# Kernel tuning notes

Hardware: AMD Instinct MI355X
Metric: run time of the kernel (lower is better)

The kernel has to match this reference:

```python
import jax, jax.numpy as jnp
import numpy as np

B, L, D, H, DH, FF = 4, 1024, 1024, 16, 64, 4096
EPS = 1e-5


def _layer_norm(x, g, b):
    m = jnp.mean(x, -1, keepdims=True)
    v = jnp.mean((x - m) ** 2, -1, keepdims=True)
    return (x - m) * jax.lax.rsqrt(v + EPS) * g + b


def setup_inputs() -> dict:
    key = jax.random.key(0)
    ks = jax.random.split(key, 20)
    s = 0.02  # param init scale
    return {
        "x": jax.random.normal(ks[0], (B, L, D), jnp.float32),
        "adj_mask_matrix": jax.random.uniform(ks[1], (B * H, L, L), jnp.float32),
        "com_mask_matrix": jax.random.uniform(ks[2], (B * H, L, L), jnp.float32),
        "lattice_rel": jax.random.normal(ks[3], (2, 1, 1, DH), jnp.float32),
        "Wq": jax.random.normal(ks[4], (D, D), jnp.float32) * s,
        "bq": jnp.zeros((D,), jnp.float32),
        "Wk": jax.random.normal(ks[5], (D, D), jnp.float32) * s,
        "bk": jnp.zeros((D,), jnp.float32),
        "Wv": jax.random.normal(ks[6], (D, D), jnp.float32) * s,
        "bv": jnp.zeros((D,), jnp.float32),
        "Wo": jax.random.normal(ks[7], (D, D), jnp.float32) * s,
        "bo": jnp.zeros((D,), jnp.float32),
        "ln1_scale": jnp.ones((D,), jnp.float32),
        "ln1_bias": jnp.zeros((D,), jnp.float32),
        "W1": jax.random.normal(ks[8], (D, FF), jnp.float32) * s,
        "b1": jnp.zeros((FF,), jnp.float32),
        "W2": jax.random.normal(ks[9], (FF, D), jnp.float32) * s,
        "b2": jnp.zeros((D,), jnp.float32),
        "ln2_scale": jnp.ones((D,), jnp.float32),
        "ln2_bias": jnp.zeros((D,), jnp.float32),
    }


def reference(x, adj_mask_matrix, com_mask_matrix, lattice_rel,
              Wq, bq, Wk, bk, Wv, bv, Wo, bo, ln1_scale, ln1_bias,
              W1, b1, W2, b2, ln2_scale, ln2_bias):
    Bsz, Ln, Dm = x.shape
    # QKV projections; flat reshape [B,L,H*dh] -> [B*H,L,dh] matches torch .view
    Q = (x @ Wq + bq).reshape(Bsz * H, Ln, DH)
    K = (x @ Wk + bk).reshape(Bsz * H, Ln, DH)
    V = (x @ Wv + bv).reshape(Bsz * H, Ln, DH)
    scale = DH ** (-0.5)
    adj_rel = lattice_rel[0]  # [1,1,dh] broadcasts over (B*H, L)
    com_rel = lattice_rel[1]
    att_adj = jnp.einsum('bqd,bkd->bqk', Q + adj_rel, K + adj_rel) * scale
    att_com = jnp.einsum('bqd,bkd->bqk', Q + com_rel, K + com_rel) * scale
    # post-softmax multiplicative masking, then sum of the two attention maps
    mask_att = (jax.nn.softmax(att_adj, axis=-1) * adj_mask_matrix
                + jax.nn.softmax(att_com, axis=-1) * com_mask_matrix)
    context = jnp.matmul(mask_att, V).reshape(Bsz, Ln, H * DH)
    out = _layer_norm(context @ Wo + bo + x, ln1_scale, ln1_bias)
    ff = jax.nn.relu(out @ W1 + b1) @ W2 + b2
    return _layer_norm(ff + out, ln2_scale, ln2_bias)
```

## Files before the change

kernel.cpp:

```cpp
#include <hip/hip_runtime.h>
#include <hip/hip_bf16.h>

typedef __attribute__((ext_vector_type(8))) short s16x8;
typedef __attribute__((ext_vector_type(4))) float f32x4;
typedef unsigned short u16;
typedef unsigned int u32;

__device__ __forceinline__ u16 f2b(float f) {
    u32 u = __float_as_uint(f);
    u32 r = (u + 0x7fffu + ((u >> 16) & 1u)) >> 16;
    return (u16)r;
}
__device__ __forceinline__ u16 bfbits(float f) {
    __hip_bfloat16 h = __float2bfloat16(f);
    return *reinterpret_cast<u16*>(&h);
}

#define MFMA16(a, b, c) __builtin_amdgcn_mfma_f32_16x16x32_bf16(a, b, c, 0, 0, 0)
#define GLDS(gp, lp)                                                              \
    __builtin_amdgcn_global_load_lds((const __attribute__((address_space(1))) void*)(gp), \
                                     (__attribute__((address_space(3))) void*)(lp), 16, 0, 0)

__global__ void k_f2b(const float* __restrict__ in, u16* __restrict__ out, int n4) {
    int i = blockIdx.x * 256 + threadIdx.x;
    if (i >= n4) return;
    float4 v = ((const float4*)in)[i];
    ushort4 o;
    o.x = f2b(v.x); o.y = f2b(v.y); o.z = f2b(v.z); o.w = f2b(v.w);
    ((ushort4*)out)[i] = o;
}

__global__ void k_wtrans(const float* __restrict__ W, u16* __restrict__ Wt, int K, int N) {
    __shared__ float t[32][33];
    int bx = blockIdx.x * 32, by = blockIdx.y * 32;
    int tx = threadIdx.x, ty = threadIdx.y;
    for (int i = 0; i < 32; i += 8)
        t[ty + i][tx] = W[(size_t)(by + ty + i) * N + bx + tx];
    __syncthreads();
    for (int i = 0; i < 32; i += 8)
        Wt[(size_t)(bx + ty + i) * K + by + tx] = f2b(t[tx][ty + i]);
}

template <int EPI>
__global__ __launch_bounds__(256) void gemm_bt(const u16* __restrict__ A, const u16* __restrict__ Bt,
                                               void* __restrict__ Cv, int M, int N, int K,
                                               const float* __restrict__ bias) {
    __shared__ __align__(16) short lA[128 * 64];
    __shared__ __align__(16) short lB[128 * 64];
    const int tid = threadIdx.x, lane = tid & 63, w = tid >> 6;
    const int l15 = lane & 15, lg = lane >> 4;
    const int bm = blockIdx.y, bn = blockIdx.x;
    const int wr = w >> 1, wc = w & 1;
    const int m0 = bm * 128, n0 = bn * 128;
    f32x4 acc[4][4] = {};

    for (int k0 = 0; k0 < K; k0 += 64) {
        #pragma unroll
        for (int i = 0; i < 4; i++) {
            int chunk = w * 4 + i;
            int arow = m0 + chunk * 8 + (lane >> 3);
            GLDS(A + (size_t)arow * K + k0 + (lane & 7) * 8, (short*)lA + chunk * 512);
            int brow = n0 + chunk * 8 + (lane >> 3);
            GLDS(Bt + (size_t)brow * K + k0 + (lane & 7) * 8, (short*)lB + chunk * 512);
        }
        __syncthreads();
        #pragma unroll
        for (int ks = 0; ks < 2; ks++) {
            s16x8 af[4], bfr[4];
            #pragma unroll
            for (int m = 0; m < 4; m++)
                af[m] = *(const s16x8*)&lA[(wr * 64 + m * 16 + l15) * 64 + ks * 32 + lg * 8];
            #pragma unroll
            for (int n = 0; n < 4; n++)
                bfr[n] = *(const s16x8*)&lB[(wc * 64 + n * 16 + l15) * 64 + ks * 32 + lg * 8];
            #pragma unroll
            for (int m = 0; m < 4; m++)
                #pragma unroll
                for (int n = 0; n < 4; n++)
                    acc[m][n] = MFMA16(af[m], bfr[n], acc[m][n]);
        }
        __syncthreads();
    }
    const int rbase = m0 + wr * 64, cbase = n0 + wc * 64;
    #pragma unroll
    for (int m = 0; m < 4; m++)
        #pragma unroll
        for (int n = 0; n < 4; n++) {
            int col = cbase + n * 16 + l15;
            int row0 = rbase + m * 16 + lg * 4;
            if (EPI == 0) {
                float* C = (float*)Cv;
                #pragma unroll
                for (int r = 0; r < 4; r++)
                    C[(size_t)(row0 + r) * N + col] = acc[m][n][r];
            } else {
                u16* C = (u16*)Cv;
                float bv = bias[col];
                #pragma unroll
                for (int r = 0; r < 4; r++)
                    C[(size_t)(row0 + r) * N + col] = bfbits(fmaxf(acc[m][n][r] + bv, 0.f));
            }
        }
}

__global__ __launch_bounds__(256) void gemm_bt64(const u16* __restrict__ A, const u16* __restrict__ Bt,
                                                 float* __restrict__ C, int M, int N, int K) {
    __shared__ __align__(16) short lA[128 * 64];
    __shared__ __align__(16) short lB[64 * 64];
    const int tid = threadIdx.x, lane = tid & 63, w = tid >> 6;
    const int l15 = lane & 15, lg = lane >> 4;
    const int m0 = blockIdx.y * 128, n0 = blockIdx.x * 64;
    f32x4 acc[2][4] = {};

    for (int k0 = 0; k0 < K; k0 += 64) {
        #pragma unroll
        for (int i = 0; i < 4; i++) {
            int chunk = w * 4 + i;
            int arow = m0 + chunk * 8 + (lane >> 3);
            GLDS(A + (size_t)arow * K + k0 + (lane & 7) * 8, (short*)lA + chunk * 512);
        }
        #pragma unroll
        for (int i = 0; i < 2; i++) {
            int chunk = w * 2 + i;
            int brow = n0 + chunk * 8 + (lane >> 3);
            GLDS(Bt + (size_t)brow * K + k0 + (lane & 7) * 8, (short*)lB + chunk * 512);
        }
        __syncthreads();
        #pragma unroll
        for (int ks = 0; ks < 2; ks++) {
            s16x8 af[2], bfr[4];
            #pragma unroll
            for (int m = 0; m < 2; m++)
                af[m] = *(const s16x8*)&lA[(w * 32 + m * 16 + l15) * 64 + ks * 32 + lg * 8];
            #pragma unroll
            for (int n = 0; n < 4; n++)
                bfr[n] = *(const s16x8*)&lB[(n * 16 + l15) * 64 + ks * 32 + lg * 8];
            #pragma unroll
            for (int m = 0; m < 2; m++)
                #pragma unroll
                for (int n = 0; n < 4; n++)
                    acc[m][n] = MFMA16(af[m], bfr[n], acc[m][n]);
        }
        __syncthreads();
    }
    #pragma unroll
    for (int m = 0; m < 2; m++)
        #pragma unroll
        for (int n = 0; n < 4; n++) {
            int col = n0 + n * 16 + l15;
            int row0 = m0 + w * 32 + m * 16 + lg * 4;
            #pragma unroll
            for (int r = 0; r < 4; r++)
                C[(size_t)(row0 + r) * N + col] = acc[m][n][r];
        }
}

__global__ void k_epi_qk2(const float* __restrict__ QKVf, int coff, const float* __restrict__ bias,
                          const float* __restrict__ rel, u16* __restrict__ Pa, u16* __restrict__ Pc, int n4) {
    int i = blockIdx.x * 256 + threadIdx.x;
    if (i >= n4) return;
    int f = i * 4;
    int row = f >> 10, col = f & 1023;
    float4 v = *(const float4*)(QKVf + (size_t)row * 3072 + coff + col);
    int d = f & 63;
    float4 b = *(const float4*)(bias + col);
    float4 r0 = *(const float4*)(rel + d);
    float4 r1 = *(const float4*)(rel + 64 + d);
    ushort4 oa, oc;
    oa.x = f2b(v.x + b.x + r0.x); oa.y = f2b(v.y + b.y + r0.y);
    oa.z = f2b(v.z + b.z + r0.z); oa.w = f2b(v.w + b.w + r0.w);
    oc.x = f2b(v.x + b.x + r1.x); oc.y = f2b(v.y + b.y + r1.y);
    oc.z = f2b(v.z + b.z + r1.z); oc.w = f2b(v.w + b.w + r1.w);
    ((ushort4*)Pa)[i] = oa;
    ((ushort4*)Pc)[i] = oc;
}

__global__ void k_vtrans2(const float* __restrict__ QKVf, const float* __restrict__ bv, u16* __restrict__ Vt) {
    __shared__ float t[64][65];
    const int g = blockIdx.y, lt = blockIdx.x;
    const int tx = threadIdx.x & 63, ty = threadIdx.x >> 6;
    const size_t gQ = (size_t)g * 65536;
    for (int i = 0; i < 64; i += 4) {
        int l = lt * 64 + ty + i;
        size_t f = gQ + (size_t)l * 64 + tx;
        t[ty + i][tx] = QKVf[(f >> 10) * 3072 + 2048 + (f & 1023)] + bv[f & 1023];
    }
    __syncthreads();
    for (int i = 0; i < 64; i += 4) {
        int d = ty + i;
        Vt[gQ + (size_t)d * 1024 + lt * 64 + tx] = f2b(t[tx][d]);
    }
}

__global__ __launch_bounds__(256) void k_attn1(const u16* __restrict__ Qa, const u16* __restrict__ Qc,
                                               const u16* __restrict__ Ka, const u16* __restrict__ Kc,
                                               const u16* __restrict__ Vt,
                                               const float* __restrict__ adjm, const float* __restrict__ comm,
                                               float* __restrict__ ctxA, float* __restrict__ ctxC) {
    const int g = blockIdx.y, qt = blockIdx.x, s = blockIdx.z;
    const u16* __restrict__ Q = s ? Qc : Qa;
    const u16* __restrict__ K = s ? Kc : Ka;
    const float* __restrict__ mask = s ? comm : adjm;
    float* __restrict__ ctxp = s ? ctxC : ctxA;

    const int tid = threadIdx.x, lane = tid & 63, w = tid >> 6;
    const int l15 = lane & 15, lg = lane >> 4;
    __shared__ __align__(16) float lE[4][16][68];

    const int q0 = qt * 64 + w * 16;
    const size_t gQ = (size_t)g * 65536;
    const float* __restrict__ mrow = mask + (size_t)g * 1048576 + (size_t)(q0 + l15) * 1024;
    const float scale = 0.125f;

    s16x8 qf[2];
    #pragma unroll
    for (int ks = 0; ks < 2; ks++)
        qf[ks] = *(const s16x8*)(Q + gQ + (size_t)(q0 + l15) * 64 + ks * 32 + lg * 8);

    f32x4 ca[4] = {};
    float la[4] = {0.f, 0.f, 0.f, 0.f};

    float4 mc[2][2], mn[2][2];
    #pragma unroll
    for (int ks = 0; ks < 2; ks++) {
        const float* p = mrow + ks * 32 + lg * 8;
        mc[ks][0] = *(const float4*)p;
        mc[ks][1] = *(const float4*)(p + 4);
    }

    #pragma unroll 2
    for (int kb = 0; kb < 1024; kb += 64) {
        const int kbn = (kb + 64) & 1023;
        #pragma unroll
        for (int ks = 0; ks < 2; ks++) {
            const float* p = mrow + kbn + ks * 32 + lg * 8;
            mn[ks][0] = *(const float4*)p;
            mn[ks][1] = *(const float4*)(p + 4);
        }
        f32x4 sa[4] = {};
        #pragma unroll
        for (int ks = 0; ks < 2; ks++)
            #pragma unroll
            for (int n = 0; n < 4; n++) {
                s16x8 kf = *(const s16x8*)(K + gQ + (size_t)(kb + n * 16 + l15) * 64 + ks * 32 + lg * 8);
                sa[n] = MFMA16(qf[ks], kf, sa[n]);
            }
        #pragma unroll
        for (int n = 0; n < 4; n++)
            #pragma unroll
            for (int r = 0; r < 4; r++) {
                float e = __expf(sa[n][r] * scale);
                la[r] += e;
                lE[w][lg * 4 + r][n * 16 + l15] = e;
            }
        #pragma unroll
        for (int ks = 0; ks < 2; ks++) {
            const float* ep = &lE[w][l15][ks * 32 + lg * 8];
            float4 e0 = *(const float4*)ep, e1 = *(const float4*)(ep + 4);
            union { s16x8 v; u16 u[8]; } pf;
            pf.u[0] = bfbits(e0.x * mc[ks][0].x); pf.u[1] = bfbits(e0.y * mc[ks][0].y);
            pf.u[2] = bfbits(e0.z * mc[ks][0].z); pf.u[3] = bfbits(e0.w * mc[ks][0].w);
            pf.u[4] = bfbits(e1.x * mc[ks][1].x); pf.u[5] = bfbits(e1.y * mc[ks][1].y);
            pf.u[6] = bfbits(e1.z * mc[ks][1].z); pf.u[7] = bfbits(e1.w * mc[ks][1].w);
            #pragma unroll
            for (int d = 0; d < 4; d++) {
                s16x8 vf = *(const s16x8*)(Vt + gQ + (size_t)(d * 16 + l15) * 1024 + kb + ks * 32 + lg * 8);
                ca[d] = MFMA16(pf.v, vf, ca[d]);
            }
        }
        #pragma unroll
        for (int ks = 0; ks < 2; ks++) {
            mc[ks][0] = mn[ks][0];
            mc[ks][1] = mn[ks][1];
        }
    }
    #pragma unroll
    for (int r = 0; r < 4; r++)
        #pragma unroll
        for (int m = 8; m >= 1; m >>= 1)
            la[r] += __shfl_xor(la[r], m);
    #pragma unroll
    for (int r = 0; r < 4; r++) {
        float il = 1.f / la[r];
        int row = q0 + lg * 4 + r;
        #pragma unroll
        for (int d = 0; d < 4; d++)
            ctxp[gQ + (size_t)row * 64 + d * 16 + l15] = ca[d][r] * il;
    }
}

__global__ void k_comb(const float* __restrict__ A, const float* __restrict__ C,
                       u16* __restrict__ out, int n4) {
    int i = blockIdx.x * 256 + threadIdx.x;
    if (i >= n4) return;
    float4 a = ((const float4*)A)[i];
    float4 c = ((const float4*)C)[i];
    ushort4 o;
    o.x = f2b(a.x + c.x); o.y = f2b(a.y + c.y);
    o.z = f2b(a.z + c.z); o.w = f2b(a.w + c.w);
    ((ushort4*)out)[i] = o;
}

__global__ __launch_bounds__(256) void k_ln(const float* __restrict__ a, const float* __restrict__ bias,
                                            const float* __restrict__ resid, const float* __restrict__ gamma,
                                            const float* __restrict__ beta, float* __restrict__ out,
                                            u16* __restrict__ outb) {
    const int row = blockIdx.x, tid = threadIdx.x;
    const size_t base = (size_t)row * 1024 + tid * 4;
    float4 av = *(const float4*)(a + base);
    float4 rv = *(const float4*)(resid + base);
    float4 bv = *(const float4*)(bias + tid * 4);
    float t0 = av.x + rv.x + bv.x, t1 = av.y + rv.y + bv.y;
    float t2 = av.z + rv.z + bv.z, t3 = av.w + rv.w + bv.w;
    __shared__ float red[4];
    float s = t0 + t1 + t2 + t3;
    #pragma unroll
    for (int m = 32; m >= 1; m >>= 1) s += __shfl_xor(s, m);
    int w = tid >> 6;
    if ((tid & 63) == 0) red[w] = s;
    __syncthreads();
    float mean = (red[0] + red[1] + red[2] + red[3]) * (1.f / 1024.f);
    float d0 = t0 - mean, d1 = t1 - mean, d2 = t2 - mean, d3 = t3 - mean;
    float q = d0 * d0 + d1 * d1 + d2 * d2 + d3 * d3;
    __syncthreads();
    #pragma unroll
    for (int m = 32; m >= 1; m >>= 1) q += __shfl_xor(q, m);
    if ((tid & 63) == 0) red[w] = q;
    __syncthreads();
    float var = (red[0] + red[1] + red[2] + red[3]) * (1.f / 1024.f);
    float rs = rsqrtf(var + 1e-5f);
    float4 gv = *(const float4*)(gamma + tid * 4);
    float4 bev = *(const float4*)(beta + tid * 4);
    float o0 = d0 * rs * gv.x + bev.x, o1 = d1 * rs * gv.y + bev.y;
    float o2 = d2 * rs * gv.z + bev.z, o3 = d3 * rs * gv.w + bev.w;
    *(float4*)(out + base) = make_float4(o0, o1, o2, o3);
    if (outb) {
        ushort4 ob;
        ob.x = f2b(o0); ob.y = f2b(o1); ob.z = f2b(o2); ob.w = f2b(o3);
        *(ushort4*)(outb + base) = ob;
    }
}

extern "C" void kernel_launch(void* const* d_in, const int* in_sizes, int n_in,
                              void* d_out, int out_size, void* d_ws, size_t ws_size,
                              hipStream_t stream) {
    const float* x    = (const float*)d_in[0];
    const float* adjm = (const float*)d_in[1];
    const float* comm = (const float*)d_in[2];
    const float* rel  = (const float*)d_in[3];
    const float* Wq   = (const float*)d_in[4];
    const float* bq   = (const float*)d_in[5];
    const float* Wk   = (const float*)d_in[6];
    const float* bk   = (const float*)d_in[7];
    const float* Wv   = (const float*)d_in[8];
    const float* bv   = (const float*)d_in[9];
    const float* Wo   = (const float*)d_in[10];
    const float* bo   = (const float*)d_in[11];
    const float* g1   = (const float*)d_in[12];
    const float* be1  = (const float*)d_in[13];
    const float* W1   = (const float*)d_in[14];
    const float* b1   = (const float*)d_in[15];
    const float* W2   = (const float*)d_in[16];
    const float* b2   = (const float*)d_in[17];
    const float* g2   = (const float*)d_in[18];
    const float* be2  = (const float*)d_in[19];
    float* out = (float*)d_out;

    char* ws = (char*)d_ws;
    const size_t MB = 1048576;
    u16*   xb    = (u16*)(ws + 0 * MB);
    u16*   Wqkvt = (u16*)(ws + 8 * MB);
    u16*   Wot   = (u16*)(ws + 14 * MB);
    u16*   W1t   = (u16*)(ws + 16 * MB);
    u16*   W2t   = (u16*)(ws + 24 * MB);
    float* QKVf  = (float*)(ws + 32 * MB);
    u16*   Qab   = (u16*)(ws + 80 * MB);
    u16*   Qcb   = (u16*)(ws + 88 * MB);
    u16*   Kab   = (u16*)(ws + 96 * MB);
    u16*   Kcb   = (u16*)(ws + 104 * MB);
    u16*   Vtb   = (u16*)(ws + 112 * MB);
    float* ctxA  = (float*)(ws + 120 * MB);
    float* ctxC  = (float*)(ws + 136 * MB);
    u16*   ctx   = (u16*)(ws + 152 * MB);
    float* ctxWo = (float*)(ws + 32 * MB);
    float* out1  = (float*)(ws + 48 * MB);
    u16*   out1b = (u16*)(ws + 64 * MB);
    u16*   rb    = (u16*)(ws + 80 * MB);
    float* ff2   = (float*)(ws + 0 * MB);

    dim3 tb(32, 8);
    k_f2b<<<4096, 256, 0, stream>>>(x, xb, 1048576);
    k_wtrans<<<dim3(32, 32), tb, 0, stream>>>(Wq, Wqkvt, 1024, 1024);
    k_wtrans<<<dim3(32, 32), tb, 0, stream>>>(Wk, Wqkvt + 1024 * 1024, 1024, 1024);
    k_wtrans<<<dim3(32, 32), tb, 0, stream>>>(Wv, Wqkvt + 2 * 1024 * 1024, 1024, 1024);
    k_wtrans<<<dim3(32, 32), tb, 0, stream>>>(Wo, Wot, 1024, 1024);
    k_wtrans<<<dim3(128, 32), tb, 0, stream>>>(W1, W1t, 1024, 4096);
    k_wtrans<<<dim3(32, 128), tb, 0, stream>>>(W2, W2t, 4096, 1024);
    gemm_bt<0><<<dim3(24, 32), 256, 0, stream>>>(xb, Wqkvt, QKVf, 4096, 3072, 1024, nullptr);
    k_epi_qk2<<<4096, 256, 0, stream>>>(QKVf, 0, bq, rel, Qab, Qcb, 1048576);
    k_epi_qk2<<<4096, 256, 0, stream>>>(QKVf, 1024, bk, rel, Kab, Kcb, 1048576);
    k_vtrans2<<<dim3(16, 64), 256, 0, stream>>>(QKVf, bv, Vtb);
    k_attn1<<<dim3(16, 64, 2), 256, 0, stream>>>(Qab, Qcb, Kab, Kcb, Vtb, adjm, comm, ctxA, ctxC);
    k_comb<<<4096, 256, 0, stream>>>(ctxA, ctxC, ctx, 1048576);
    gemm_bt64<<<dim3(16, 32), 256, 0, stream>>>(ctx, Wot, ctxWo, 4096, 1024, 1024);
    k_ln<<<4096, 256, 0, stream>>>(ctxWo, bo, x, g1, be1, out1, out1b);
    gemm_bt<1><<<dim3(32, 32), 256, 0, stream>>>(out1b, W1t, rb, 4096, 4096, 1024, b1);
    gemm_bt64<<<dim3(16, 32), 256, 0, stream>>>(rb, W2t, ff2, 4096, 1024, 4096);
    k_ln<<<4096, 256, 0, stream>>>(ff2, b2, out1, g2, be2, out, nullptr);
}
```

Baseline: 657.7 us.

## Split attention into QK-exp and masked PV kernels with bf16 score buffer

Splits the fused attention kernel into two passes per branch. The first computes exp(QK^T) and row sums, storing exp scores as bf16 in a 128MB workspace. The second reads them back, applies the fp32 mask, and runs the PV MFMA. The second branch's PV pass folds in the adj/com sum and bf16 conversion, removing the separate combine kernel. It also remaps block ids so heads are grouped per XCD. The aim is to decouple mask streaming from the QK compute, but it adds a large round trip of score traffic and extra bf16 rounding of the exp values.

Measured after the change: 670.6 us. About the same (+1.9%).

```diff
diff --git a/kernel.cpp b/kernel.cpp
--- a/kernel.cpp
+++ b/kernel.cpp
@@ -14,6 +14,9 @@
 __device__ __forceinline__ u16 bfbits(float f) {
     __hip_bfloat16 h = __float2bfloat16(f);
     return *reinterpret_cast<u16*>(&h);
+}
+__device__ __forceinline__ float b2f(u16 b) {
+    return __uint_as_float(((u32)b) << 16);
 }
 
 #define MFMA16(a, b, c) __builtin_amdgcn_mfma_f32_16x16x32_bf16(a, b, c, 0, 0, 0)
@@ -192,24 +195,18 @@
     }
 }
 
-__global__ __launch_bounds__(256) void k_attn1(const u16* __restrict__ Qa, const u16* __restrict__ Qc,
-                                               const u16* __restrict__ Ka, const u16* __restrict__ Kc,
-                                               const u16* __restrict__ Vt,
-                                               const float* __restrict__ adjm, const float* __restrict__ comm,
-                                               float* __restrict__ ctxA, float* __restrict__ ctxC) {
-    const int g = blockIdx.y, qt = blockIdx.x, s = blockIdx.z;
-    const u16* __restrict__ Q = s ? Qc : Qa;
-    const u16* __restrict__ K = s ? Kc : Ka;
-    const float* __restrict__ mask = s ? comm : adjm;
-    float* __restrict__ ctxp = s ? ctxC : ctxA;
-
+__global__ __launch_bounds__(256) void k_qke(const u16* __restrict__ Q, const u16* __restrict__ K,
+                                             u16* __restrict__ E, float* __restrict__ denom) {
+    const int bid = blockIdx.x;
+    const int xcd = bid & 7, j = bid >> 3;
+    const int g = xcd * 8 + (j & 7), qt = j >> 3;
     const int tid = threadIdx.x, lane = tid & 63, w = tid >> 6;
     const int l15 = lane & 15, lg = lane >> 4;
     __shared__ __align__(16) float lE[4][16][68];
 
     const int q0 = qt * 64 + w * 16;
     const size_t gQ = (size_t)g * 65536;
-    const float* __restrict__ mrow = mask + (size_t)g * 1048576 + (size_t)(q0 + l15) * 1024;
+    const size_t ebase = ((((size_t)g * 16 + qt) * 4 + w) * 16384) + (size_t)lane * 8;
     const float scale = 0.125f;
 
     s16x8 qf[2];
@@ -217,26 +214,11 @@
     for (int ks = 0; ks < 2; ks++)
         qf[ks] = *(const s16x8*)(Q + gQ + (size_t)(q0 + l15) * 64 + ks * 32 + lg * 8);
 
-    f32x4 ca[4] = {};
     float la[4] = {0.f, 0.f, 0.f, 0.f};
 
-    float4 mc[2][2], mn[2][2];
-    #pragma unroll
-    for (int ks = 0; ks < 2; ks++) {
-        const float* p = mrow + ks * 32 + lg * 8;
-        mc[ks][0] = *(const float4*)p;
-        mc[ks][1] = *(const float4*)(p + 4);
-    }
-
-    #pragma unroll 2
-    for (int kb = 0; kb < 1024; kb += 64) {
-        const int kbn = (kb + 64) & 1023;
-        #pragma unroll
-        for (int ks = 0; ks < 2; ks++) {
-            const float* p = mrow + kbn + ks * 32 + lg * 8;
-            mn[ks][0] = *(const float4*)p;
-            mn[ks][1] = *(const float4*)(p + 4);
-        }
+    #pragma unroll 1
+    for (int it = 0; it < 16; it++) {
+        const int kb = it * 64;
         f32x4 sa[4] = {};
         #pragma unroll
         for (int ks = 0; ks < 2; ks++)
@@ -257,48 +239,89 @@
         for (int ks = 0; ks < 2; ks++) {
             const float* ep = &lE[w][l15][ks * 32 + lg * 8];
             float4 e0 = *(const float4*)ep, e1 = *(const float4*)(ep + 4);
+            uint4 st;
+            st.x = (u32)f2b(e0.x) | ((u32)f2b(e0.y) << 16);
+            st.y = (u32)f2b(e0.z) | ((u32)f2b(e0.w) << 16);
+            st.z = (u32)f2b(e1.x) | ((u32)f2b(e1.y) << 16);
+            st.w = (u32)f2b(e1.z) | ((u32)f2b(e1.w) << 16);
+            *(uint4*)(E + ebase + (size_t)it * 1024 + ks * 512) = st;
+        }
+    }
+    #pragma unroll
+    for (int r = 0; r < 4; r++)
+        #pragma unroll
+        for (int m = 8; m >= 1; m >>= 1)
+            la[r] += __shfl_xor(la[r], m);
+    if (l15 == 0) {
+        #pragma unroll
+        for (int r = 0; r < 4; r++)
+            denom[g * 1024 + q0 + lg * 4 + r] = la[r];
+    }
+}
+
+template <int PHASE>
+__global__ __launch_bounds__(256) void k_pv(const u16* __restrict__ E, const u16* __restrict__ Vt,
+                                            const float* __restrict__ mask, const float* __restrict__ denom,
+                                            float* __restrict__ ctxP, u16* __restrict__ ctx) {
+    const int bid = blockIdx.x;
+    const int xcd = bid & 7, j = bid >> 3;
+    const int g = xcd * 8 + (j & 7), qt = j >> 3;
+    const int tid = threadIdx.x, lane = tid & 63, w = tid >> 6;
+    const int l15 = lane & 15, lg = lane >> 4;
+
+    const int q0 = qt * 64 + w * 16;
+    const size_t gQ = (size_t)g * 65536;
+    const float* __restrict__ mrow = mask + (size_t)g * 1048576 + (size_t)(q0 + l15) * 1024 + lg * 8;
+    const size_t ebase = ((((size_t)g * 16 + qt) * 4 + w) * 16384) + (size_t)lane * 8;
+
+    f32x4 ca[4] = {};
+
+    #pragma unroll 2
+    for (int it = 0; it < 16; it++) {
+        const int kb = it * 64;
+        s16x8 ev[2];
+        float4 m0[2], m1[2];
+        #pragma unroll
+        for (int ks = 0; ks < 2; ks++) {
+            ev[ks] = *(const s16x8*)(E + ebase + (size_t)it * 1024 + ks * 512);
+            m0[ks] = *(const float4*)(mrow + kb + ks * 32);
+            m1[ks] = *(const float4*)(mrow + kb + ks * 32 + 4);
+        }
+        #pragma unroll
+        for (int ks = 0; ks < 2; ks++) {
             union { s16x8 v; u16 u[8]; } pf;
-            pf.u[0] = bfbits(e0.x * mc[ks][0].x); pf.u[1] = bfbits(e0.y * mc[ks][0].y);
-            pf.u[2] = bfbits(e0.z * mc[ks][0].z); pf.u[3] = bfbits(e0.w * mc[ks][0].w);
-            pf.u[4] = bfbits(e1.x * mc[ks][1].x); pf.u[5] = bfbits(e1.y * mc[ks][1].y);
-            pf.u[6] = bfbits(e1.z * mc[ks][1].z); pf.u[7] = bfbits(e1.w * mc[ks][1].w);
+            pf.u[0] = f2b(b2f((u16)ev[ks][0]) * m0[ks].x);
+            pf.u[1] = f2b(b2f((u16)ev[ks][1]) * m0[ks].y);
+            pf.u[2] = f2b(b2f((u16)ev[ks][2]) * m0[ks].z);
+            pf.u[3] = f2b(b2f((u16)ev[ks][3]) * m0[ks].w);
+            pf.u[4] = f2b(b2f((u16)ev[ks][4]) * m1[ks].x);
+            pf.u[5] = f2b(b2f((u16)ev[ks][5]) * m1[ks].y);
+            pf.u[6] = f2b(b2f((u16)ev[ks][6]) * m1[ks].z);
+            pf.u[7] = f2b(b2f((u16)ev[ks][7]) * m1[ks].w);
             #pragma unroll
             for (int d = 0; d < 4; d++) {
                 s16x8 vf = *(const s16x8*)(Vt + gQ + (size_t)(d * 16 + l15) * 1024 + kb + ks * 32 + lg * 8);
                 ca[d] = MFMA16(pf.v, vf, ca[d]);
             }
         }
-        #pragma unroll
-        for (int ks = 0; ks < 2; ks++) {
-            mc[ks][0] = mn[ks][0];
-            mc[ks][1] = mn[ks][1];
-        }
-    }
+    }
+    float il[4];
     #pragma unroll
     for (int r = 0; r < 4; r++)
-        #pragma unroll
-        for (int m = 8; m >= 1; m >>= 1)
-            la[r] += __shfl_xor(la[r], m);
+        il[r] = 1.f / denom[g * 1024 + q0 + lg * 4 + r];
     #pragma unroll
     for (int r = 0; r < 4; r++) {
-        float il = 1.f / la[r];
         int row = q0 + lg * 4 + r;
         #pragma unroll
-        for (int d = 0; d < 4; d++)
-            ctxp[gQ + (size_t)row * 64 + d * 16 + l15] = ca[d][r] * il;
-    }
-}
-
-__global__ void k_comb(const float* __restrict__ A, const float* __restrict__ C,
-                       u16* __restrict__ out, int n4) {
-    int i = blockIdx.x * 256 + threadIdx.x;
-    if (i >= n4) return;
-    float4 a = ((const float4*)A)[i];
-    float4 c = ((const float4*)C)[i];
-    ushort4 o;
-    o.x = f2b(a.x + c.x); o.y = f2b(a.y + c.y);
-    o.z = f2b(a.z + c.z); o.w = f2b(a.w + c.w);
-    ((ushort4*)out)[i] = o;
+        for (int d = 0; d < 4; d++) {
+            size_t idx = gQ + (size_t)row * 64 + d * 16 + l15;
+            if (PHASE == 0) {
+                ctxP[idx] = ca[d][r] * il[r];
+            } else {
+                ctx[idx] = f2b(ctxP[idx] + ca[d][r] * il[r]);
+            }
+        }
+    }
 }
 
 __global__ __launch_bounds__(256) void k_ln(const float* __restrict__ a, const float* __restrict__ bias,
@@ -379,9 +402,11 @@
     u16*   Kab   = (u16*)(ws + 96 * MB);
     u16*   Kcb   = (u16*)(ws + 104 * MB);
     u16*   Vtb   = (u16*)(ws + 112 * MB);
-    float* ctxA  = (float*)(ws + 120 * MB);
-    float* ctxC  = (float*)(ws + 136 * MB);
-    u16*   ctx   = (u16*)(ws + 152 * MB);
+    u16*   Eb    = (u16*)(ws + 120 * MB);
+    float* denA  = (float*)(ws + 248 * MB);
+    float* denC  = denA + 65536;
+    float* ctxP  = (float*)(ws + 249 * MB);
+    u16*   ctx   = (u16*)(ws + 265 * MB);
     float* ctxWo = (float*)(ws + 32 * MB);
     float* out1  = (float*)(ws + 48 * MB);
     u16*   out1b = (u16*)(ws + 64 * MB);
@@ -400,8 +425,10 @@
     k_epi_qk2<<<4096, 256, 0, stream>>>(QKVf, 0, bq, rel, Qab, Qcb, 1048576);
     k_epi_qk2<<<4096, 256, 0, stream>>>(QKVf, 1024, bk, rel, Kab, Kcb, 1048576);
     k_vtrans2<<<dim3(16, 64), 256, 0, stream>>>(QKVf, bv, Vtb);
-    k_attn1<<<dim3(16, 64, 2), 256, 0, stream>>>(Qab, Qcb, Kab, Kcb, Vtb, adjm, comm, ctxA, ctxC);
-    k_comb<<<4096, 256, 0, stream>>>(ctxA, ctxC, ctx, 1048576);
+    k_qke<<<1024, 256, 0, stream>>>(Qab, Kab, Eb, denA);
+    k_pv<0><<<1024, 256, 0, stream>>>(Eb, Vtb, adjm, denA, ctxP, nullptr);
+    k_qke<<<1024, 256, 0, stream>>>(Qcb, Kcb, Eb, denC);
+    k_pv<1><<<1024, 256, 0, stream>>>(Eb, Vtb, comm, denC, ctxP, ctx);
     gemm_bt64<<<dim3(16, 32), 256, 0, stream>>>(ctx, Wot, ctxWo, 4096, 1024, 1024);
     k_ln<<<4096, 256, 0, stream>>>(ctxWo, bo, x, g1, be1, out1, out1b);
     gemm_bt<1><<<dim3(32, 32), 256, 0, stream>>>(out1b, W1t, rb, 4096, 4096, 1024, b1);
```

## Fuse QKV bias/rel/transpose epilogue into GEMM and restructure attention loads

Applied to the files above, without the earlier changes.

Moves the Q/K bias plus lattice-rel add, the bf16 conversion and the V transpose into the QKV GEMM epilogue. This removes the fp32 QKV intermediate and three follow-up kernels. The attention kernel now batches its K, V and mask loads at the start of each iteration, separated by sched barriers, in place of the previous mask double-buffering. It also remaps block indices so that blocks sharing a head group land on the same XCD. The fused V-transpose path writes scattered 2-byte stores, and the new load batching raises register pressure in attention.

Result: faster. 600.0 us (-8.8%).

```diff
diff --git a/kernel.cpp b/kernel.cpp
--- a/kernel.cpp
+++ b/kernel.cpp
@@ -11,15 +11,12 @@
     u32 r = (u + 0x7fffu + ((u >> 16) & 1u)) >> 16;
     return (u16)r;
 }
-__device__ __forceinline__ u16 bfbits(float f) {
-    __hip_bfloat16 h = __float2bfloat16(f);
-    return *reinterpret_cast<u16*>(&h);
-}
 
 #define MFMA16(a, b, c) __builtin_amdgcn_mfma_f32_16x16x32_bf16(a, b, c, 0, 0, 0)
 #define GLDS(gp, lp)                                                              \
     __builtin_amdgcn_global_load_lds((const __attribute__((address_space(1))) void*)(gp), \
                                      (__attribute__((address_space(3))) void*)(lp), 16, 0, 0)
+#define SB() __builtin_amdgcn_sched_barrier(0)
 
 __global__ void k_f2b(const float* __restrict__ in, u16* __restrict__ out, int n4) {
     int i = blockIdx.x * 256 + threadIdx.x;
@@ -41,6 +38,87 @@
         Wt[(size_t)(bx + ty + i) * K + by + tx] = f2b(t[tx][ty + i]);
 }
 
+__global__ __launch_bounds__(256) void gemm_qkv(const u16* __restrict__ A, const u16* __restrict__ Bt,
+                                                const float* __restrict__ bq, const float* __restrict__ bk,
+                                                const float* __restrict__ bv, const float* __restrict__ rel,
+                                                u16* __restrict__ Qa, u16* __restrict__ Qc,
+                                                u16* __restrict__ Ka, u16* __restrict__ Kc,
+                                                u16* __restrict__ Vt) {
+    __shared__ __align__(16) short lA[128 * 64];
+    __shared__ __align__(16) short lB[128 * 64];
+    const int tid = threadIdx.x, lane = tid & 63, w = tid >> 6;
+    const int l15 = lane & 15, lg = lane >> 4;
+    const int wr = w >> 1, wc = w & 1;
+    const int m0 = blockIdx.y * 128, n0 = blockIdx.x * 128;
+    const int KK = 1024;
+    f32x4 acc[4][4] = {};
+
+    for (int k0 = 0; k0 < KK; k0 += 64) {
+        #pragma unroll
+        for (int i = 0; i < 4; i++) {
+            int chunk = w * 4 + i;
+            int arow = m0 + chunk * 8 + (lane >> 3);
+            GLDS(A + (size_t)arow * KK + k0 + (lane & 7) * 8, (short*)lA + chunk * 512);
+            int brow = n0 + chunk * 8 + (lane >> 3);
+            GLDS(Bt + (size_t)brow * KK + k0 + (lane & 7) * 8, (short*)lB + chunk * 512);
+        }
+        __syncthreads();
+        #pragma unroll
+        for (int ks = 0; ks < 2; ks++) {
+            s16x8 af[4], bfr[4];
+            #pragma unroll
+            for (int m = 0; m < 4; m++)
+                af[m] = *(const s16x8*)&lA[(wr * 64 + m * 16 + l15) * 64 + ks * 32 + lg * 8];
+            #pragma unroll
+            for (int n = 0; n < 4; n++)
+                bfr[n] = *(const s16x8*)&lB[(wc * 64 + n * 16 + l15) * 64 + ks * 32 + lg * 8];
+            #pragma unroll
+            for (int m = 0; m < 4; m++)
+                #pragma unroll
+                for (int n = 0; n < 4; n++)
+                    acc[m][n] = MFMA16(af[m], bfr[n], acc[m][n]);
+        }
+        __syncthreads();
+    }
+    const int rbase = m0 + wr * 64, cbase = n0 + wc * 64;
+    const int seg = cbase >> 10;
+    #pragma unroll
+    for (int m = 0; m < 4; m++)
+        #pragma unroll
+        for (int n = 0; n < 4; n++) {
+            int col = cbase + n * 16 + l15;
+            int c1 = col & 1023, d = col & 63;
+            int row0 = rbase + m * 16 + lg * 4;
+            if (seg == 0) {
+                float bb = bq[c1], r0 = rel[d], r1 = rel[64 + d];
+                #pragma unroll
+                for (int r = 0; r < 4; r++) {
+                    float v = acc[m][n][r] + bb;
+                    size_t o = (size_t)(row0 + r) * 1024 + c1;
+                    Qa[o] = f2b(v + r0);
+                    Qc[o] = f2b(v + r1);
+                }
+            } else if (seg == 1) {
+                float bb = bk[c1], r0 = rel[d], r1 = rel[64 + d];
+                #pragma unroll
+                for (int r = 0; r < 4; r++) {
+                    float v = acc[m][n][r] + bb;
+                    size_t o = (size_t)(row0 + r) * 1024 + c1;
+                    Ka[o] = f2b(v + r0);
+                    Kc[o] = f2b(v + r1);
+                }
+            } else {
+                float bb = bv[c1];
+                #pragma unroll
+                for (int r = 0; r < 4; r++) {
+                    int row = row0 + r;
+                    size_t o = (size_t)(row >> 6) * 65536 + (size_t)d * 1024 + (row & 63) * 16 + (c1 >> 6);
+                    Vt[o] = f2b(acc[m][n][r] + bb);
+                }
+            }
+        }
+}
+
 template <int EPI>
 __global__ __launch_bounds__(256) void gemm_bt(const u16* __restrict__ A, const u16* __restrict__ Bt,
                                                void* __restrict__ Cv, int M, int N, int K,
@@ -49,9 +127,8 @@
     __shared__ __align__(16) short lB[128 * 64];
     const int tid = threadIdx.x, lane = tid & 63, w = tid >> 6;
     const int l15 = lane & 15, lg = lane >> 4;
-    const int bm = blockIdx.y, bn = blockIdx.x;
     const int wr = w >> 1, wc = w & 1;
-    const int m0 = bm * 128, n0 = bn * 128;
+    const int m0 = blockIdx.y * 128, n0 = blockIdx.x * 128;
     f32x4 acc[4][4] = {};
 
     for (int k0 = 0; k0 < K; k0 += 64) {
@@ -88,18 +165,11 @@
         for (int n = 0; n < 4; n++) {
             int col = cbase + n * 16 + l15;
             int row0 = rbase + m * 16 + lg * 4;
-            if (EPI == 0) {
-                float* C = (float*)Cv;
-                #pragma unroll
-                for (int r = 0; r < 4; r++)
-                    C[(size_t)(row0 + r) * N + col] = acc[m][n][r];
-            } else {
-                u16* C = (u16*)Cv;
-                float bv = bias[col];
-                #pragma unroll
-                for (int r = 0; r < 4; r++)
-                    C[(size_t)(row0 + r) * N + col] = bfbits(fmaxf(acc[m][n][r] + bv, 0.f));
-            }
+            u16* C = (u16*)Cv;
+            float bv = bias[col];
+            #pragma unroll
+            for (int r = 0; r < 4; r++)
+                C[(size_t)(row0 + r) * N + col] = f2b(fmaxf(acc[m][n][r] + bv, 0.f));
         }
 }
 
@@ -155,49 +225,15 @@
         }
 }
 
-__global__ void k_epi_qk2(const float* __restrict__ QKVf, int coff, const float* __restrict__ bias,
-                          const float* __restrict__ rel, u16* __restrict__ Pa, u16* __restrict__ Pc, int n4) {
-    int i = blockIdx.x * 256 + threadIdx.x;
-    if (i >= n4) return;
-    int f = i * 4;
-    int row = f >> 10, col = f & 1023;
-    float4 v = *(const float4*)(QKVf + (size_t)row * 3072 + coff + col);
-    int d = f & 63;
-    float4 b = *(const float4*)(bias + col);
-    float4 r0 = *(const float4*)(rel + d);
-    float4 r1 = *(const float4*)(rel + 64 + d);
-    ushort4 oa, oc;
-    oa.x = f2b(v.x + b.x + r0.x); oa.y = f2b(v.y + b.y + r0.y);
-    oa.z = f2b(v.z + b.z + r0.z); oa.w = f2b(v.w + b.w + r0.w);
-    oc.x = f2b(v.x + b.x + r1.x); oc.y = f2b(v.y + b.y + r1.y);
-    oc.z = f2b(v.z + b.z + r1.z); oc.w = f2b(v.w + b.w + r1.w);
-    ((ushort4*)Pa)[i] = oa;
-    ((ushort4*)Pc)[i] = oc;
-}
-
-__global__ void k_vtrans2(const float* __restrict__ QKVf, const float* __restrict__ bv, u16* __restrict__ Vt) {
-    __shared__ float t[64][65];
-    const int g = blockIdx.y, lt = blockIdx.x;
-    const int tx = threadIdx.x & 63, ty = threadIdx.x >> 6;
-    const size_t gQ = (size_t)g * 65536;
-    for (int i = 0; i < 64; i += 4) {
-        int l = lt * 64 + ty + i;
-        size_t f = gQ + (size_t)l * 64 + tx;
-        t[ty + i][tx] = QKVf[(f >> 10) * 3072 + 2048 + (f & 1023)] + bv[f & 1023];
-    }
-    __syncthreads();
-    for (int i = 0; i < 64; i += 4) {
-        int d = ty + i;
-        Vt[gQ + (size_t)d * 1024 + lt * 64 + tx] = f2b(t[tx][d]);
-    }
-}
-
-__global__ __launch_bounds__(256) void k_attn1(const u16* __restrict__ Qa, const u16* __restrict__ Qc,
+__global__ __launch_bounds__(256) void k_attnf(const u16* __restrict__ Qa, const u16* __restrict__ Qc,
                                                const u16* __restrict__ Ka, const u16* __restrict__ Kc,
                                                const u16* __restrict__ Vt,
                                                const float* __restrict__ adjm, const float* __restrict__ comm,
                                                float* __restrict__ ctxA, float* __restrict__ ctxC) {
-    const int g = blockIdx.y, qt = blockIdx.x, s = blockIdx.z;
+    const int bid = blockIdx.x;
+    const int xcd = bid & 7, j = bid >> 3;
+    const int g = xcd * 8 + (j & 7), qt = j >> 3;
+    const int s = blockIdx.z;
     const u16* __restrict__ Q = s ? Qc : Qa;
     const u16* __restrict__ K = s ? Kc : Ka;
     const float* __restrict__ mask = s ? comm : adjm;
@@ -209,7 +245,7 @@
 
     const int q0 = qt * 64 + w * 16;
     const size_t gQ = (size_t)g * 65536;
-    const float* __restrict__ mrow = mask + (size_t)g * 1048576 + (size_t)(q0 + l15) * 1024;
+    const float* __restrict__ mrow = mask + (size_t)g * 1048576 + (size_t)(q0 + l15) * 1024 + lg * 8;
     const float scale = 0.125f;
 
     s16x8 qf[2];
@@ -220,31 +256,35 @@
     f32x4 ca[4] = {};
     float la[4] = {0.f, 0.f, 0.f, 0.f};
 
-    float4 mc[2][2], mn[2][2];
-    #pragma unroll
-    for (int ks = 0; ks < 2; ks++) {
-        const float* p = mrow + ks * 32 + lg * 8;
-        mc[ks][0] = *(const float4*)p;
-        mc[ks][1] = *(const float4*)(p + 4);
-    }
-
-    #pragma unroll 2
-    for (int kb = 0; kb < 1024; kb += 64) {
-        const int kbn = (kb + 64) & 1023;
+    #pragma unroll 1
+    for (int it = 0; it < 16; it++) {
+        const int kb = it * 64;
+        s16x8 kf[8];
+        #pragma unroll
+        for (int ks = 0; ks < 2; ks++)
+            #pragma unroll
+            for (int n = 0; n < 4; n++)
+                kf[ks * 4 + n] = *(const s16x8*)(K + gQ + (size_t)(kb + n * 16 + l15) * 64 + ks * 32 + lg * 8);
+        SB();
+        s16x8 vf[8];
+        float4 mf[4];
+        #pragma unroll
+        for (int ks = 0; ks < 2; ks++)
+            #pragma unroll
+            for (int d = 0; d < 4; d++)
+                vf[ks * 4 + d] = *(const s16x8*)(Vt + gQ + (size_t)(d * 16 + l15) * 1024 + kb + ks * 32 + lg * 8);
         #pragma unroll
         for (int ks = 0; ks < 2; ks++) {
-            const float* p = mrow + kbn + ks * 32 + lg * 8;
-            mn[ks][0] = *(const float4*)p;
-            mn[ks][1] = *(const float4*)(p + 4);
-        }
+            mf[ks * 2 + 0] = *(const float4*)(mrow + kb + ks * 32);
+            mf[ks * 2 + 1] = *(const float4*)(mrow + kb + ks * 32 + 4);
+        }
+        SB();
         f32x4 sa[4] = {};
         #pragma unroll
         for (int ks = 0; ks < 2; ks++)
             #pragma unroll
-            for (int n = 0; n < 4; n++) {
-                s16x8 kf = *(const s16x8*)(K + gQ + (size_t)(kb + n * 16 + l15) * 64 + ks * 32 + lg * 8);
-                sa[n] = MFMA16(qf[ks], kf, sa[n]);
-            }
+            for (int n = 0; n < 4; n++)
+                sa[n] = MFMA16(qf[ks], kf[ks * 4 + n], sa[n]);
         #pragma unroll
         for (int n = 0; n < 4; n++)
             #pragma unroll
@@ -258,21 +298,15 @@
             const float* ep = &lE[w][l15][ks * 32 + lg * 8];
             float4 e0 = *(const float4*)ep, e1 = *(const float4*)(ep + 4);
             union { s16x8 v; u16 u[8]; } pf;
-            pf.u[0] = bfbits(e0.x * mc[ks][0].x); pf.u[1] = bfbits(e0.y * mc[ks][0].y);
-            pf.u[2] = bfbits(e0.z * mc[ks][0].z); pf.u[3] = bfbits(e0.w * mc[ks][0].w);
-            pf.u[4] = bfbits(e1.x * mc[ks][1].x); pf.u[5] = bfbits(e1.y * mc[ks][1].y);
-            pf.u[6] = bfbits(e1.z * mc[ks][1].z); pf.u[7] = bfbits(e1.w * mc[ks][1].w);
-            #pragma unroll
-            for (int d = 0; d < 4; d++) {
-                s16x8 vf = *(const s16x8*)(Vt + gQ + (size_t)(d * 16 + l15) * 1024 + kb + ks * 32 + lg * 8);
-                ca[d] = MFMA16(pf.v, vf, ca[d]);
-            }
-        }
-        #pragma unroll
-        for (int ks = 0; ks < 2; ks++) {
-            mc[ks][0] = mn[ks][0];
-            mc[ks][1] = mn[ks][1];
-        }
+            pf.u[0] = f2b(e0.x * mf[ks * 2].x); pf.u[1] = f2b(e0.y * mf[ks * 2].y);
+            pf.u[2] = f2b(e0.z * mf[ks * 2].z); pf.u[3] = f2b(e0.w * mf[ks * 2].w);
+            pf.u[4] = f2b(e1.x * mf[ks * 2 + 1].x); pf.u[5] = f2b(e1.y * mf[ks * 2 + 1].y);
+            pf.u[6] = f2b(e1.z * mf[ks * 2 + 1].z); pf.u[7] = f2b(e1.w * mf[ks * 2 + 1].w);
+            #pragma unroll
+            for (int d = 0; d < 4; d++)
+                ca[d] = MFMA16(pf.v, vf[ks * 4 + d], ca[d]);
+        }
+        SB();
     }
     #pragma unroll
     for (int r = 0; r < 4; r++)
@@ -373,19 +407,18 @@
     u16*   Wot   = (u16*)(ws + 14 * MB);
     u16*   W1t   = (u16*)(ws + 16 * MB);
     u16*   W2t   = (u16*)(ws + 24 * MB);
-    float* QKVf  = (float*)(ws + 32 * MB);
-    u16*   Qab   = (u16*)(ws + 80 * MB);
-    u16*   Qcb   = (u16*)(ws + 88 * MB);
-    u16*   Kab   = (u16*)(ws + 96 * MB);
-    u16*   Kcb   = (u16*)(ws + 104 * MB);
-    u16*   Vtb   = (u16*)(ws + 112 * MB);
-    float* ctxA  = (float*)(ws + 120 * MB);
-    float* ctxC  = (float*)(ws + 136 * MB);
-    u16*   ctx   = (u16*)(ws + 152 * MB);
+    u16*   Qab   = (u16*)(ws + 32 * MB);
+    u16*   Qcb   = (u16*)(ws + 40 * MB);
+    u16*   Kab   = (u16*)(ws + 48 * MB);
+    u16*   Kcb   = (u16*)(ws + 56 * MB);
+    u16*   Vtb   = (u16*)(ws + 64 * MB);
+    float* ctxA  = (float*)(ws + 72 * MB);
+    float* ctxC  = (float*)(ws + 88 * MB);
+    u16*   ctx   = (u16*)(ws + 104 * MB);
     float* ctxWo = (float*)(ws + 32 * MB);
     float* out1  = (float*)(ws + 48 * MB);
     u16*   out1b = (u16*)(ws + 64 * MB);
-    u16*   rb    = (u16*)(ws + 80 * MB);
+    u16*   rb    = (u16*)(ws + 72 * MB);
     float* ff2   = (float*)(ws + 0 * MB);
 
     dim3 tb(32, 8);
@@ -396,11 +429,9 @@
     k_wtrans<<<dim3(32, 32), tb, 0, stream>>>(Wo, Wot, 1024, 1024);
     k_wtrans<<<dim3(128, 32), tb, 0, stream>>>(W1, W1t, 1024, 4096);
     k_wtrans<<<dim3(32, 128), tb, 0, stream>>>(W2, W2t, 4096, 1024);
-    gemm_bt<0><<<dim3(24, 32), 256, 0, stream>>>(xb, Wqkvt, QKVf, 4096, 3072, 1024, nullptr);
-    k_epi_qk2<<<4096, 256, 0, stream>>>(QKVf, 0, bq, rel, Qab, Qcb, 1048576);
-    k_epi_qk2<<<4096, 256, 0, stream>>>(QKVf, 1024, bk, rel, Kab, Kcb, 1048576);
-    k_vtrans2<<<dim3(16, 64), 256, 0, stream>>>(QKVf, bv, Vtb);
-    k_attn1<<<dim3(16, 64, 2), 256, 0, stream>>>(Qab, Qcb, Kab, Kcb, Vtb, adjm, comm, ctxA, ctxC);
+    gemm_qkv<<<dim3(24, 32), 256, 0, stream>>>(xb, Wqkvt, bq, bk, bv, rel,
+                                               Qab, Qcb, Kab, Kcb, Vtb);
+    k_attnf<<<dim3(1024, 1, 2), 256, 0, stream>>>(Qab, Qcb, Kab, Kcb, Vtb, adjm, comm, ctxA, ctxC);
     k_comb<<<4096, 256, 0, stream>>>(ctxA, ctxC, ctx, 1048576);
     gemm_bt64<<<dim3(16, 32), 256, 0, stream>>>(ctx, Wot, ctxWo, 4096, 1024, 1024);
     k_ln<<<4096, 256, 0, stream>>>(ctxWo, bo, x, g1, be1, out1, out1b);
```
